# Kernel tuning notes

Hardware: AMD Instinct MI355X
Metric: run time of the kernel (lower is better)

## Reference

```python
import jax, jax.numpy as jnp
import numpy as np

N_NODES = 50000
N_EDGES = 1600000
F_IN = 64
C = 128
NOUT = 3
N_LAYERS = 3  # 1 encoder EGNN + 2 decoder EGNN


def setup_inputs() -> dict:
    key = jax.random.key(0)
    ks = jax.random.split(key, 16)
    s = lambda k, shp, scale: jax.random.normal(k, shp, dtype=jnp.float32) * scale
    inp = {
        'src': jax.random.randint(ks[0], (N_EDGES,), 0, N_NODES),
        'dst': jax.random.randint(ks[1], (N_EDGES,), 0, N_NODES),
        'node_attr': jax.random.normal(ks[2], (N_NODES, F_IN), dtype=jnp.float32),
        'xyz': jax.random.normal(ks[3], (N_NODES, 3), dtype=jnp.float32),
        'emb_w1': s(ks[4], (F_IN, C), F_IN ** -0.5),
        'emb_b1': jnp.zeros((C,), jnp.float32),
        'ln1_g': jnp.ones((C,), jnp.float32),
        'ln1_b': jnp.zeros((C,), jnp.float32),
        'emb_w2': s(ks[5], (C, C), C ** -0.5),
        'emb_b2': jnp.zeros((C,), jnp.float32),
        'ln2_g': jnp.ones((C,), jnp.float32),
        'ln2_b': jnp.zeros((C,), jnp.float32),
        'e_w1': s(ks[6], (N_LAYERS, 2 * C + 1, C), (2 * C + 1) ** -0.5),
        'e_b1': jnp.zeros((N_LAYERS, C), jnp.float32),
        'e_w2': s(ks[7], (N_LAYERS, C, C), C ** -0.5),
        'e_b2': jnp.zeros((N_LAYERS, C), jnp.float32),
        'n_w1': s(ks[8], (N_LAYERS, 2 * C, C), (2 * C) ** -0.5),
        'n_b1': jnp.zeros((N_LAYERS, C), jnp.float32),
        'n_w2': s(ks[9], (N_LAYERS, C, C), C ** -0.5),
        'n_b2': jnp.zeros((N_LAYERS, C), jnp.float32),
        'c_w1': s(ks[10], (N_LAYERS, C, C), C ** -0.5),
        'c_b1': jnp.zeros((N_LAYERS, C), jnp.float32),
        'c_w2': s(ks[11], (N_LAYERS, C, 1), 0.01),  # small coord head as in EGNN practice
        'dec_ln_g': jnp.ones((C,), jnp.float32),
        'dec_ln_b': jnp.zeros((C,), jnp.float32),
        'out_w': s(ks[12], (C, NOUT), C ** -0.5),
        'out_b': jnp.zeros((NOUT,), jnp.float32),
    }
    return inp


def _layer_norm(x, g, b, eps=1e-5):
    mu = x.mean(-1, keepdims=True)
    var = ((x - mu) ** 2).mean(-1, keepdims=True)
    return (x - mu) * jax.lax.rsqrt(var + eps) * g + b


def _egnn_layer(h, x, src, dst, ew1, eb1, ew2, eb2, nw1, nb1, nw2, nb2, cw1, cb1, cw2):
    # DGL EGNNConv: messages src -> dst, sum aggregation.
    n = h.shape[0]
    x_diff = x[src] - x[dst]                               # [E, 3]
    radial = (x_diff * x_diff).sum(-1, keepdims=True)      # [E, 1]
    x_diff = x_diff / (jnp.sqrt(radial) + 1e-30)           # normalized diff
    f = jnp.concatenate([h[src], h[dst], radial], axis=-1)  # [E, 2C+1]
    m = jax.nn.silu(f @ ew1 + eb1)
    m = jax.nn.silu(m @ ew2 + eb2)                          # msg_h [E, C]
    cm = jax.nn.silu(m @ cw1 + cb1) @ cw2                   # [E, 1]
    msg_x = cm * x_diff                                     # [E, 3]
    h_agg = jax.ops.segment_sum(m, dst, num_segments=n)
    x_agg = jax.ops.segment_sum(msg_x, dst, num_segments=n)
    h_new = jnp.concatenate([h, h_agg], axis=-1)
    h_new = jax.nn.silu(h_new @ nw1 + nb1) @ nw2 + nb2
    return h_new, x + x_agg


def reference(src, dst, node_attr, xyz,
              emb_w1, emb_b1, ln1_g, ln1_b, emb_w2, emb_b2, ln2_g, ln2_b,
              e_w1, e_b1, e_w2, e_b2, n_w1, n_b1, n_w2, n_b2,
              c_w1, c_b1, c_w2, dec_ln_g, dec_ln_b, out_w, out_b):
    gelu = lambda t: jax.nn.gelu(t, approximate=False)  # torch nn.GELU default (erf)
    # initial node embedding (eval mode: dropout = identity)
    h = gelu(_layer_norm(node_attr @ emb_w1 + emb_b1, ln1_g, ln1_b))
    h = gelu(_layer_norm(h @ emb_w2 + emb_b2, ln2_g, ln2_b))
    # encoder GraphConv: 1 EGNN layer, coord output discarded
    h, _ = _egnn_layer(h, xyz, src, dst,
                       e_w1[0], e_b1[0], e_w2[0], e_b2[0],
                       n_w1[0], n_b1[0], n_w2[0], n_b2[0],
                       c_w1[0], c_b1[0], c_w2[0])
    # decoder EquivalentTransformer: 2 EGNN layers starting again from xyz
    coord = xyz
    for i in (1, 2):
        h, coord = _egnn_layer(h, coord, src, dst,
                               e_w1[i], e_b1[i], e_w2[i], e_b2[i],
                               n_w1[i], n_b1[i], n_w2[i], n_b2[i],
                               c_w1[i], c_b1[i], c_w2[i])
        h = _layer_norm(gelu(h), dec_ln_g, dec_ln_b)
    return h @ out_w + out_b  # [N, nout]
```

## Files before the change

kernel.cpp:

```cpp
#include <hip/hip_runtime.h>
#include <hip/hip_fp16.h>
#include <math.h>

#define NN 50000
#define NE 1600000
#define CC 128
#define FIN 64

typedef __attribute__((ext_vector_type(8))) _Float16 half8;
typedef __attribute__((ext_vector_type(2))) __fp16 fp16x2;
typedef __attribute__((ext_vector_type(4))) float f32x4;

__device__ __forceinline__ f32x4 mfma16f(half8 a, half8 b, f32x4 c) {
  return __builtin_amdgcn_mfma_f32_16x16x32_f16(a, b, c, 0, 0, 0);
}

__device__ __forceinline__ float silu_f(float x) {
  return x * __builtin_amdgcn_rcpf(1.0f + __expf(-x));
}
__device__ __forceinline__ float gelu_f(float x) { return 0.5f * x * (1.0f + erff(x * 0.7071067811865475f)); }

__device__ __forceinline__ unsigned pkrtz(float a, float b) {
  fp16x2 h = __builtin_amdgcn_cvt_pkrtz(a, b);
  return *(unsigned*)&h;
}

__device__ __forceinline__ float hsum32(float v) {
  v += __shfl_xor(v, 16);
  v += __shfl_xor(v, 8);
  v += __shfl_xor(v, 4);
  v += __shfl_xor(v, 2);
  v += __shfl_xor(v, 1);
  return v;
}

__device__ __forceinline__ float hsum8(float v) {
  v += __shfl_xor(v, 4);
  v += __shfl_xor(v, 2);
  v += __shfl_xor(v, 1);
  return v;
}

__global__ __launch_bounds__(256)
void hist_kernel(const int* __restrict__ dst, int* __restrict__ cnt)
{
  const int i = blockIdx.x * 256 + threadIdx.x;
  if (i < NE) atomicAdd(&cnt[dst[i]], 1);
}

__global__ __launch_bounds__(1024)
void scan_kernel(const int* __restrict__ cnt, int* __restrict__ next)
{
  __shared__ int part[1024];
  const int tid = threadIdx.x;
  const int per = (NN + 1023) / 1024;
  const int base = tid * per;
  int s = 0;
  for (int i = 0; i < per; ++i) {
    const int n = base + i;
    if (n < NN) s += cnt[n];
  }
  part[tid] = s;
  __syncthreads();
  if (tid == 0) {
    int acc = 0;
    for (int i = 0; i < 1024; ++i) { const int t = part[i]; part[i] = acc; acc += t; }
  }
  __syncthreads();
  int off = part[tid];
  for (int i = 0; i < per; ++i) {
    const int n = base + i;
    if (n < NN) { next[n] = off; off += cnt[n]; }
  }
}

__global__ __launch_bounds__(256)
void slot_kernel(const int* __restrict__ dst, int* __restrict__ next, int* __restrict__ perm)
{
  const int i = blockIdx.x * 256 + threadIdx.x;
  if (i < NE) perm[atomicAdd(&next[dst[i]], 1)] = i;
}

__global__ __launch_bounds__(256)
void wt_split(const float* __restrict__ W, __half* __restrict__ Wh, __half* __restrict__ Wl,
              const int K, const int layers, const int strideIn)
{
  const int gid = blockIdx.x * 256 + threadIdx.x;
  if (gid >= layers * 128 * K) return;
  const int l = gid / (128 * K);
  const int rem = gid - l * 128 * K;
  const int n = rem / K;
  const int k = rem - n * K;
  const float w = W[(size_t)l * strideIn + (size_t)k * 128 + n];
  const __half hi = __float2half(w);
  Wh[gid] = hi;
  Wl[gid] = __float2half(w - __half2float(hi));
}

__global__ __launch_bounds__(256)
void pq_kernel(const __half* __restrict__ h_hi,
               const __half* __restrict__ W1h, const __half* __restrict__ W1l,
               const float* __restrict__ eb1, __half* __restrict__ PQ)
{
  __shared__ __align__(16) __half ah[32 * 128];
  const int tid = threadIdx.x;
  const int n0 = blockIdx.x * 32;
  {
    const int row = tid >> 3, sub = tid & 7;
    int n = n0 + row; if (n >= NN) n = NN - 1;
    #pragma unroll
    for (int t = 0; t < 2; ++t) {
      const int c8 = sub * 2 + t;
      const uint4 v = *(const uint4*)(h_hi + (size_t)n * CC + c8 * 8);
      *(uint4*)(ah + row * 128 + ((c8 ^ (row & 15)) * 8)) = v;
    }
  }
  __syncthreads();

  const int lane = tid & 63;
  const int li = lane & 15, quad = lane >> 4;
  const int wv = tid >> 6;
  const int c0 = wv * 32 + li, c1 = c0 + 16;

  f32x4 acc[2][4];
  {
    const float b0 = eb1[c0], b1 = eb1[c1];
    acc[0][0] = acc[1][0] = (f32x4){b0, b0, b0, b0};
    acc[0][1] = acc[1][1] = (f32x4){b1, b1, b1, b1};
    acc[0][2] = acc[1][2] = (f32x4){0, 0, 0, 0};
    acc[0][3] = acc[1][3] = (f32x4){0, 0, 0, 0};
  }
  const __half* bp[4] = { W1h + (size_t)c0 * 256, W1h + (size_t)c1 * 256,
                          W1h + (size_t)c0 * 256 + 128, W1h + (size_t)c1 * 256 + 128 };
  const __half* lp[4] = { W1l + (size_t)c0 * 256, W1l + (size_t)c1 * 256,
                          W1l + (size_t)c0 * 256 + 128, W1l + (size_t)c1 * 256 + 128 };
  #pragma unroll
  for (int ks = 0; ks < 4; ++ks) {
    const int ko = ks * 32 + quad * 8;
    half8 Bh[4], Bl[4];
    #pragma unroll
    for (int o = 0; o < 4; ++o) { Bh[o] = *(const half8*)(bp[o] + ko); Bl[o] = *(const half8*)(lp[o] + ko); }
    #pragma unroll
    for (int mi = 0; mi < 2; ++mi) {
      const half8 A = *(const half8*)(ah + (mi * 16 + li) * 128 + (((ks * 4 + quad) ^ li) * 8));
      #pragma unroll
      for (int o = 0; o < 4; ++o) {
        acc[mi][o] = mfma16f(A, Bh[o], acc[mi][o]);
        acc[mi][o] = mfma16f(A, Bl[o], acc[mi][o]);
      }
    }
  }
  const int cmap[4] = { c0, c1, 128 + c0, 128 + c1 };
  #pragma unroll
  for (int mi = 0; mi < 2; ++mi) {
    #pragma unroll
    for (int r = 0; r < 4; ++r) {
      const int n = n0 + mi * 16 + quad * 4 + r;
      if (n < NN) {
        __half* po = PQ + (size_t)n * 256;
        #pragma unroll
        for (int o = 0; o < 4; ++o) po[cmap[o]] = __float2half(acc[mi][o][r]);
      }
    }
  }
}

template<int COORD>
__global__ __launch_bounds__(512)
void edge_kernel(const int* __restrict__ perm,
                 const int* __restrict__ src, const int* __restrict__ dst,
                 const __half* __restrict__ PQ, const float* __restrict__ xyz,
                 const float* __restrict__ w1rad,
                 const __half* __restrict__ W2h, const __half* __restrict__ W2l,
                 const float* __restrict__ eb2,
                 const __half* __restrict__ W3h, const __half* __restrict__ W3l,
                 const float* __restrict__ cb1, const float* __restrict__ cw2,
                 float* __restrict__ h_agg, float* __restrict__ x_agg)
{
  const int EPB = 128;
  __shared__ __align__(16) unsigned char smem[128 * 132 * 2];
  __shared__ int sidx[EPB], didx[EPB];
  __shared__ float radial[EPB];
  __shared__ float xdn[COORD ? EPB : 1][3];
  __shared__ float sx[COORD ? EPB : 1];
  __shared__ float cw2s[COORD ? 128 : 1];

  __half* ab = (__half*)smem;
  __half* tbuf = (__half*)smem;

  const int tid = threadIdx.x;
  const size_t ebase = (size_t)blockIdx.x * EPB;

  if (tid < EPB) {
    const int e = perm[ebase + tid];
    const int s = src[e], d = dst[e];
    sidx[tid] = s; didx[tid] = d;
    const float* xs = xyz + (size_t)s * 3;
    const float* xd = xyz + (size_t)d * 3;
    const float dx = xs[0] - xd[0], dy = xs[1] - xd[1], dz = xs[2] - xd[2];
    const float r = dx * dx + dy * dy + dz * dz;
    radial[tid] = r;
    if (COORD) {
      const float inv = __builtin_amdgcn_rcpf(sqrtf(r) + 1e-30f);
      xdn[tid][0] = dx * inv; xdn[tid][1] = dy * inv; xdn[tid][2] = dz * inv;
    }
  }
  if (COORD && tid >= 128 && tid < 256) cw2s[tid - 128] = cw2[tid - 128];
  __syncthreads();

  {
    const int e = tid >> 2, q = tid & 3, c = q * 32;
    const float r = radial[e];
    const __half* prow = PQ + (size_t)sidx[e] * 256 + c;
    const __half* qrow = PQ + (size_t)didx[e] * 256 + 128 + c;
    #pragma unroll
    for (int i = 0; i < 4; ++i) {
      union { uint4 u; __half2 h2[4]; } pu, qu;
      pu.u = *(const uint4*)(prow + i * 8);
      qu.u = *(const uint4*)(qrow + i * 8);
      const float4 wa = *(const float4*)(w1rad + c + i * 8);
      const float4 wb = *(const float4*)(w1rad + c + i * 8 + 4);
      const float wf[8] = { wa.x, wa.y, wa.z, wa.w, wb.x, wb.y, wb.z, wb.w };
      float v[8];
      #pragma unroll
      for (int j = 0; j < 4; ++j) {
        const float2 p = __half22float2(pu.h2[j]);
        const float2 qq = __half22float2(qu.h2[j]);
        v[2 * j]     = silu_f(p.x + qq.x + r * wf[2 * j]);
        v[2 * j + 1] = silu_f(p.y + qq.y + r * wf[2 * j + 1]);
      }
      uint4 H;
      H.x = pkrtz(v[0], v[1]); H.y = pkrtz(v[2], v[3]);
      H.z = pkrtz(v[4], v[5]); H.w = pkrtz(v[6], v[7]);
      *(uint4*)(ab + e * 128 + (((q * 4 + i) ^ (e & 15)) * 8)) = H;
    }
  }
  __syncthreads();

  const int lane = tid & 63;
  const int li = lane & 15, quad = lane >> 4;
  const int wv = tid >> 6;
  const int c0 = wv * 16 + li;

  f32x4 mm[8];
  {
    const float b0 = eb2[c0];
    #pragma unroll
    for (int mi = 0; mi < 8; ++mi) mm[mi] = (f32x4){b0, b0, b0, b0};
  }
  {
    const __half* bh0 = W2h + (size_t)c0 * 128 + quad * 8;
    const __half* bl0 = W2l + (size_t)c0 * 128 + quad * 8;
    #pragma unroll
    for (int ks = 0; ks < 4; ++ks) {
      const half8 Bh0 = *(const half8*)(bh0 + ks * 32);
      const half8 Bl0 = *(const half8*)(bl0 + ks * 32);
      #pragma unroll
      for (int mi = 0; mi < 8; ++mi) {
        const half8 A = *(const half8*)(ab + (mi * 16 + li) * 128 + (((ks * 4 + quad) ^ li) * 8));
        mm[mi] = mfma16f(A, Bh0, mm[mi]);
        mm[mi] = mfma16f(A, Bl0, mm[mi]);
      }
    }
  }
  #pragma unroll
  for (int mi = 0; mi < 8; ++mi) {
    #pragma unroll
    for (int r = 0; r < 4; ++r) mm[mi][r] = silu_f(mm[mi][r]);
  }
  __syncthreads();

  if (!COORD) {
    #pragma unroll
    for (int mi = 0; mi < 8; ++mi) {
      #pragma unroll
      for (int r = 0; r < 4; ++r)
        tbuf[(mi * 16 + quad * 4 + r) * 132 + c0] = __float2half(mm[mi][r]);
    }
    __syncthreads();
    const int c = tid & 127, grp = tid >> 7;
    const int j0 = grp * 32, j1 = j0 + 32;
    float ss = 0.0f;
    for (int j = j0; j < j1; ++j) {
      ss += __half2float(tbuf[j * 132 + c]);
      const int dj = didx[j];
      if (j == j1 - 1 || didx[j + 1] != dj) {
        atomicAdd(&h_agg[(size_t)dj * CC + c], ss);
        ss = 0.0f;
      }
    }
  } else {
    #pragma unroll
    for (int mi = 0; mi < 8; ++mi) {
      #pragma unroll
      for (int r = 0; r < 4; ++r) {
        const int row = mi * 16 + quad * 4 + r;
        ab[row * 128 + (((c0 >> 3) ^ (row & 15)) * 8) + (c0 & 7)] = __float2half(mm[mi][r]);
      }
    }
    __syncthreads();
    {
      const int c = tid & 127, grp = tid >> 7;
      const int j0 = grp * 32, j1 = j0 + 32;
      float ss = 0.0f;
      for (int j = j0; j < j1; ++j) {
        ss += __half2float(ab[j * 128 + (((c >> 3) ^ (j & 15)) * 8) + (c & 7)]);
        const int dj = didx[j];
        if (j == j1 - 1 || didx[j + 1] != dj) {
          atomicAdd(&h_agg[(size_t)dj * CC + c], ss);
          ss = 0.0f;
        }
      }
    }
    f32x4 tt[8];
    {
      const float b0 = cb1[c0];
      #pragma unroll
      for (int mi = 0; mi < 8; ++mi) tt[mi] = (f32x4){b0, b0, b0, b0};
    }
    {
      const __half* bh0 = W3h + (size_t)c0 * 128 + quad * 8;
      const __half* bl0 = W3l + (size_t)c0 * 128 + quad * 8;
      #pragma unroll
      for (int ks = 0; ks < 4; ++ks) {
        const half8 Bh0 = *(const half8*)(bh0 + ks * 32);
        const half8 Bl0 = *(const half8*)(bl0 + ks * 32);
        #pragma unroll
        for (int mi = 0; mi < 8; ++mi) {
          const half8 A = *(const half8*)(ab + (mi * 16 + li) * 128 + (((ks * 4 + quad) ^ li) * 8));
          tt[mi] = mfma16f(A, Bh0, tt[mi]);
          tt[mi] = mfma16f(A, Bl0, tt[mi]);
        }
      }
    }
    __syncthreads();
    #pragma unroll
    for (int mi = 0; mi < 8; ++mi) {
      #pragma unroll
      for (int r = 0; r < 4; ++r)
        tbuf[(mi * 16 + quad * 4 + r) * 132 + c0] = __float2half(silu_f(tt[mi][r]));
    }
    __syncthreads();
    if (tid < EPB) {
      float ss = 0.0f;
      #pragma unroll 8
      for (int k = 0; k < CC; ++k) ss += __half2float(tbuf[tid * 132 + k]) * cw2s[k];
      sx[tid] = ss;
    }
    __syncthreads();
    if (tid < 12) {
      const int c = tid >> 2, grp = tid & 3;
      const int j0 = grp * 32, j1 = j0 + 32;
      float a = 0.0f;
      for (int j = j0; j < j1; ++j) {
        a += sx[j] * xdn[j][c];
        const int dj = didx[j];
        if (j == j1 - 1 || didx[j + 1] != dj) {
          atomicAdd(&x_agg[(size_t)dj * 3 + c], a);
          a = 0.0f;
        }
      }
    }
  }
}

__global__ __launch_bounds__(256)
void node_mfma(const __half* __restrict__ h_hi, const __half* __restrict__ h_lo,
               const float* __restrict__ h_agg,
               const __half* __restrict__ NW1h, const __half* __restrict__ NW1l,
               const float* __restrict__ nb1,
               const __half* __restrict__ NW2h, const __half* __restrict__ NW2l,
               const float* __restrict__ nb2,
               __half* __restrict__ ho_hi, __half* __restrict__ ho_lo, const int post_ln,
               const float* __restrict__ lng, const float* __restrict__ lnb,
               const int do_coord, const float* __restrict__ xin,
               const float* __restrict__ x_agg, float* __restrict__ coord_out)
{
  __shared__ __align__(16) __half ab[32 * 256];
  __shared__ __align__(16) __half ab2[32 * 128];
  __shared__ float cbuf[32 * 132];

  const int tid = threadIdx.x;
  const int n0 = blockIdx.x * 32;

  {
    const int row = tid >> 3, q = tid & 7;
    int n = n0 + row; if (n >= NN) n = NN - 1;
    #pragma unroll
    for (int t = 0; t < 2; ++t) {
      const int c8 = q * 2 + t;
      const uint4 v = *(const uint4*)(h_hi + (size_t)n * CC + c8 * 8);
      *(uint4*)(ab + row * 256 + ((c8 ^ (row & 15)) * 8)) = v;
    }
    #pragma unroll
    for (int t = 0; t < 2; ++t) {
      const int c8 = 16 + q * 2 + t;
      const float4 a0 = *(const float4*)(h_agg + (size_t)n * CC + (q * 2 + t) * 8);
      const float4 a1 = *(const float4*)(h_agg + (size_t)n * CC + (q * 2 + t) * 8 + 4);
      uint4 H;
      H.x = pkrtz(a0.x, a0.y); H.y = pkrtz(a0.z, a0.w);
      H.z = pkrtz(a1.x, a1.y); H.w = pkrtz(a1.z, a1.w);
      *(uint4*)(ab + row * 256 + ((c8 ^ (row & 15)) * 8)) = H;
    }
  }
  if (do_coord && tid < 96) {
    const int n = n0 + tid / 3, d = tid % 3;
    if (n < NN)
      coord_out[(size_t)n * 3 + d] = xin[(size_t)n * 3 + d] + x_agg[(size_t)n * 3 + d];
  }
  __syncthreads();

  const int lane = tid & 63;
  const int li = lane & 15, quad = lane >> 4;
  const int wv = tid >> 6;

  f32x4 a1[2][2];
  {
    const float b0 = nb1[wv * 32 + li], b1 = nb1[wv * 32 + 16 + li];
    a1[0][0] = a1[1][0] = (f32x4){b0, b0, b0, b0};
    a1[0][1] = a1[1][1] = (f32x4){b1, b1, b1, b1};
  }
  {
    const __half* b0h = NW1h + (size_t)(wv * 32 + li) * 256 + quad * 8;
    const __half* b0l = NW1l + (size_t)(wv * 32 + li) * 256 + quad * 8;
    const __half* b1h = NW1h + (size_t)(wv * 32 + 16 + li) * 256 + quad * 8;
    const __half* b1l = NW1l + (size_t)(wv * 32 + 16 + li) * 256 + quad * 8;
    #pragma unroll
    for (int ks = 0; ks < 8; ++ks) {
      const half8 Bh0 = *(const half8*)(b0h + ks * 32);
      const half8 Bl0 = *(const half8*)(b0l + ks * 32);
      const half8 Bh1 = *(const half8*)(b1h + ks * 32);
      const half8 Bl1 = *(const half8*)(b1l + ks * 32);
      #pragma unroll
      for (int mi = 0; mi < 2; ++mi) {
        const half8 A = *(const half8*)(ab + (mi * 16 + li) * 256 + (((ks * 4 + quad) ^ li) * 8));
        a1[mi][0] = mfma16f(A, Bh0, a1[mi][0]);
        a1[mi][0] = mfma16f(A, Bl0, a1[mi][0]);
        a1[mi][1] = mfma16f(A, Bh1, a1[mi][1]);
        a1[mi][1] = mfma16f(A, Bl1, a1[mi][1]);
      }
    }
  }
  #pragma unroll
  for (int mi = 0; mi < 2; ++mi) {
    #pragma unroll
    for (int nc = 0; nc < 2; ++nc) {
      const int col = wv * 32 + nc * 16 + li;
      #pragma unroll
      for (int r = 0; r < 4; ++r) {
        const int row = mi * 16 + quad * 4 + r;
        ab2[row * 128 + (((col >> 3) ^ (row & 15)) * 8) + (col & 7)] =
            __float2half(silu_f(a1[mi][nc][r]));
      }
    }
  }
  __syncthreads();

  f32x4 a2[2][2];
  {
    const float b0 = nb2[wv * 32 + li], b1 = nb2[wv * 32 + 16 + li];
    a2[0][0] = a2[1][0] = (f32x4){b0, b0, b0, b0};
    a2[0][1] = a2[1][1] = (f32x4){b1, b1, b1, b1};
  }
  {
    const __half* b0h = NW2h + (size_t)(wv * 32 + li) * 128 + quad * 8;
    const __half* b0l = NW2l + (size_t)(wv * 32 + li) * 128 + quad * 8;
    const __half* b1h = NW2h + (size_t)(wv * 32 + 16 + li) * 128 + quad * 8;
    const __half* b1l = NW2l + (size_t)(wv * 32 + 16 + li) * 128 + quad * 8;
    #pragma unroll
    for (int ks = 0; ks < 4; ++ks) {
      const half8 Bh0 = *(const half8*)(b0h + ks * 32);
      const half8 Bl0 = *(const half8*)(b0l + ks * 32);
      const half8 Bh1 = *(const half8*)(b1h + ks * 32);
      const half8 Bl1 = *(const half8*)(b1l + ks * 32);
      #pragma unroll
      for (int mi = 0; mi < 2; ++mi) {
        const half8 A = *(const half8*)(ab2 + (mi * 16 + li) * 128 + (((ks * 4 + quad) ^ li) * 8));
        a2[mi][0] = mfma16f(A, Bh0, a2[mi][0]);
        a2[mi][0] = mfma16f(A, Bl0, a2[mi][0]);
        a2[mi][1] = mfma16f(A, Bh1, a2[mi][1]);
        a2[mi][1] = mfma16f(A, Bl1, a2[mi][1]);
      }
    }
  }
  #pragma unroll
  for (int mi = 0; mi < 2; ++mi) {
    #pragma unroll
    for (int nc = 0; nc < 2; ++nc) {
      const int col = wv * 32 + nc * 16 + li;
      #pragma unroll
      for (int r = 0; r < 4; ++r)
        cbuf[(mi * 16 + quad * 4 + r) * 132 + col] = a2[mi][nc][r];
    }
  }
  __syncthreads();

  {
    const int row = tid >> 3, q = tid & 7;
    const int n = n0 + row;
    float v[16];
    #pragma unroll
    for (int i = 0; i < 16; ++i) v[i] = cbuf[row * 132 + q * 16 + i];
    if (post_ln) {
      float s = 0.0f;
      #pragma unroll
      for (int i = 0; i < 16; ++i) { v[i] = gelu_f(v[i]); s += v[i]; }
      const float mu = hsum8(s) * (1.0f / 128.0f);
      float vs = 0.0f;
      #pragma unroll
      for (int i = 0; i < 16; ++i) { v[i] -= mu; vs += v[i] * v[i]; }
      const float rs = rsqrtf(hsum8(vs) * (1.0f / 128.0f) + 1e-5f);
      #pragma unroll
      for (int i = 0; i < 16; ++i)
        v[i] = v[i] * rs * lng[q * 16 + i] + lnb[q * 16 + i];
    }
    if (n < NN) {
      __half h[16], l[16];
      #pragma unroll
      for (int i = 0; i < 16; ++i) {
        h[i] = __float2half(v[i]);
        l[i] = __float2half(v[i] - __half2float(h[i]));
      }
      #pragma unroll
      for (int t = 0; t < 2; ++t) {
        *(uint4*)(ho_hi + (size_t)n * CC + q * 16 + t * 8) = *(uint4*)(h + t * 8);
        *(uint4*)(ho_lo + (size_t)n * CC + q * 16 + t * 8) = *(uint4*)(l + t * 8);
      }
    }
  }
}

template<int K, int ROWS>
__device__ __forceinline__ void mm_tile(const float* __restrict__ fb, const int fstride,
                                        const float* __restrict__ W, const float* __restrict__ bias,
                                        const int c0, const int r0, float (&acc)[ROWS][4])
{
  const float4 b = *(const float4*)(bias + c0);
  #pragma unroll
  for (int i = 0; i < ROWS; ++i) { acc[i][0] = b.x; acc[i][1] = b.y; acc[i][2] = b.z; acc[i][3] = b.w; }
  #pragma unroll 2
  for (int k = 0; k < K; k += 4) {
    const float4 w0 = *(const float4*)(W + (size_t)(k + 0) * CC + c0);
    const float4 w1 = *(const float4*)(W + (size_t)(k + 1) * CC + c0);
    const float4 w2 = *(const float4*)(W + (size_t)(k + 2) * CC + c0);
    const float4 w3 = *(const float4*)(W + (size_t)(k + 3) * CC + c0);
    #pragma unroll
    for (int i = 0; i < ROWS; ++i) {
      const float4 f = *(const float4*)(fb + (r0 + i) * fstride + k);
      acc[i][0] += f.x * w0.x + f.y * w1.x + f.z * w2.x + f.w * w3.x;
      acc[i][1] += f.x * w0.y + f.y * w1.y + f.z * w2.y + f.w * w3.y;
      acc[i][2] += f.x * w0.z + f.y * w1.z + f.z * w2.z + f.w * w3.z;
      acc[i][3] += f.x * w0.w + f.y * w1.w + f.z * w2.w + f.w * w3.w;
    }
  }
}

__device__ __forceinline__ void ln_then_gelu(float (&v)[4], const float* __restrict__ g,
                                             const float* __restrict__ b, const int c0)
{
  const float mu = hsum32(v[0] + v[1] + v[2] + v[3]) * (1.0f / 128.0f);
  const float d0 = v[0] - mu, d1 = v[1] - mu, d2 = v[2] - mu, d3 = v[3] - mu;
  const float var = hsum32(d0 * d0 + d1 * d1 + d2 * d2 + d3 * d3) * (1.0f / 128.0f);
  const float rs = rsqrtf(var + 1e-5f);
  const float4 gv = *(const float4*)(g + c0);
  const float4 bv = *(const float4*)(b + c0);
  v[0] = gelu_f(d0 * rs * gv.x + bv.x);
  v[1] = gelu_f(d1 * rs * gv.y + bv.y);
  v[2] = gelu_f(d2 * rs * gv.z + bv.z);
  v[3] = gelu_f(d3 * rs * gv.w + bv.w);
}

__device__ __forceinline__ void store_hilo4(__half* __restrict__ hi, __half* __restrict__ lo,
                                            const float v0, const float v1,
                                            const float v2, const float v3)
{
  __half h[4], l[4];
  h[0] = __float2half(v0); h[1] = __float2half(v1); h[2] = __float2half(v2); h[3] = __float2half(v3);
  l[0] = __float2half(v0 - __half2float(h[0]));
  l[1] = __float2half(v1 - __half2float(h[1]));
  l[2] = __float2half(v2 - __half2float(h[2]));
  l[3] = __float2half(v3 - __half2float(h[3]));
  *(ushort4*)hi = *(ushort4*)h;
  *(ushort4*)lo = *(ushort4*)l;
}

__global__ __launch_bounds__(256)
void embed_kernel(const float* __restrict__ na,
                  const float* __restrict__ w1, const float* __restrict__ b1,
                  const float* __restrict__ g1, const float* __restrict__ be1,
                  const float* __restrict__ w2, const float* __restrict__ b2,
                  const float* __restrict__ g2, const float* __restrict__ be2,
                  __half* __restrict__ ho_hi, __half* __restrict__ ho_lo)
{
  const int AS = 68, MS = 132;
  __shared__ float ain[16 * AS];
  __shared__ float hb[16 * MS];
  const int tid = threadIdx.x;
  const size_t n0 = (size_t)blockIdx.x * 16;
  {
    const int n = tid >> 4, q = tid & 15;
    *(float4*)(ain + n * AS + q * 4) = *(const float4*)(na + (n0 + n) * FIN + q * 4);
  }
  __syncthreads();
  const int cg = tid & 31, ng = tid >> 5;
  const int c0 = cg * 4, m0 = ng * 2;
  float acc[2][4];
  mm_tile<64, 2>(ain, AS, w1, b1, c0, m0, acc);
  #pragma unroll
  for (int i = 0; i < 2; ++i) {
    ln_then_gelu(acc[i], g1, be1, c0);
    *(float4*)(hb + (m0 + i) * MS + c0) = make_float4(acc[i][0], acc[i][1], acc[i][2], acc[i][3]);
  }
  __syncthreads();
  float acc2[2][4];
  mm_tile<128, 2>(hb, MS, w2, b2, c0, m0, acc2);
  #pragma unroll
  for (int i = 0; i < 2; ++i) {
    ln_then_gelu(acc2[i], g2, be2, c0);
    store_hilo4(ho_hi + (n0 + m0 + i) * CC + c0, ho_lo + (n0 + m0 + i) * CC + c0,
                acc2[i][0], acc2[i][1], acc2[i][2], acc2[i][3]);
  }
}

__global__ __launch_bounds__(192)
void out_kernel(const __half* __restrict__ h_hi, const __half* __restrict__ h_lo,
                const float* __restrict__ w, const float* __restrict__ b,
                float* __restrict__ out)
{
  const int gid = blockIdx.x * 192 + threadIdx.x;
  if (gid >= NN * 3) return;
  const int n = gid / 3, j = gid % 3;
  float acc = b[j];
  const __half* hh = h_hi + (size_t)n * CC;
  const __half* hl = h_lo + (size_t)n * CC;
  #pragma unroll 4
  for (int k = 0; k < CC; ++k) acc += (__half2float(hh[k]) + __half2float(hl[k])) * w[k * 3 + j];
  out[gid] = acc;
}

extern "C" void kernel_launch(void* const* d_in, const int* in_sizes, int n_in,
                              void* d_out, int out_size, void* d_ws, size_t ws_size,
                              hipStream_t stream)
{
  (void)in_sizes; (void)n_in; (void)out_size; (void)ws_size;
  const int*   src       = (const int*)d_in[0];
  const int*   dst       = (const int*)d_in[1];
  const float* node_attr = (const float*)d_in[2];
  const float* xyz       = (const float*)d_in[3];
  const float* emb_w1    = (const float*)d_in[4];
  const float* emb_b1    = (const float*)d_in[5];
  const float* ln1_g     = (const float*)d_in[6];
  const float* ln1_b     = (const float*)d_in[7];
  const float* emb_w2    = (const float*)d_in[8];
  const float* emb_b2    = (const float*)d_in[9];
  const float* ln2_g     = (const float*)d_in[10];
  const float* ln2_b     = (const float*)d_in[11];
  const float* e_w1      = (const float*)d_in[12];
  const float* e_b1      = (const float*)d_in[13];
  const float* e_w2      = (const float*)d_in[14];
  const float* e_b2      = (const float*)d_in[15];
  const float* n_w1      = (const float*)d_in[16];
  const float* n_b1      = (const float*)d_in[17];
  const float* n_w2      = (const float*)d_in[18];
  const float* n_b2      = (const float*)d_in[19];
  const float* c_w1      = (const float*)d_in[20];
  const float* c_b1      = (const float*)d_in[21];
  const float* c_w2      = (const float*)d_in[22];
  const float* dec_ln_g  = (const float*)d_in[23];
  const float* dec_ln_b  = (const float*)d_in[24];
  const float* out_w     = (const float*)d_in[25];
  const float* out_b     = (const float*)d_in[26];

  char* wsb = (char*)d_ws;
  float*  h_agg = (float*)wsb;                      wsb += (size_t)NN * CC * 4;
  __half* PQ    = (__half*)wsb;                     wsb += (size_t)NN * 256 * 2;
  float*  x_agg = (float*)wsb;                      wsb += (size_t)NN * 3 * 4;
  float*  coord = (float*)wsb;                      wsb += (size_t)NN * 3 * 4;
  __half* h_hi  = (__half*)wsb;                     wsb += (size_t)NN * CC * 2;
  __half* h_lo  = (__half*)wsb;                     wsb += (size_t)NN * CC * 2;
  __half* W1h   = (__half*)wsb;                     wsb += (size_t)3 * 128 * 256 * 2;
  __half* W1l   = (__half*)wsb;                     wsb += (size_t)3 * 128 * 256 * 2;
  __half* W2h   = (__half*)wsb;                     wsb += (size_t)3 * 128 * 128 * 2;
  __half* W2l   = (__half*)wsb;                     wsb += (size_t)3 * 128 * 128 * 2;
  __half* W3h   = (__half*)wsb;                     wsb += (size_t)128 * 128 * 2;
  __half* W3l   = (__half*)wsb;                     wsb += (size_t)128 * 128 * 2;
  __half* NW1h  = (__half*)wsb;                     wsb += (size_t)3 * 128 * 256 * 2;
  __half* NW1l  = (__half*)wsb;                     wsb += (size_t)3 * 128 * 256 * 2;
  __half* NW2h  = (__half*)wsb;                     wsb += (size_t)3 * 128 * 128 * 2;
  __half* NW2l  = (__half*)wsb;                     wsb += (size_t)3 * 128 * 128 * 2;
  int*    permA = (int*)wsb;                        wsb += (size_t)NE * 4;
  int*    cnt   = (int*)wsb;                        wsb += (size_t)NN * 4;
  int*    nextA = (int*)wsb;                        wsb += (size_t)NN * 4;
  float*  out   = (float*)d_out;

  const int NGRID = NN / 16;
  const int N32GRID = (NN + 31) / 32;
  const int EGRID = NE / 128;

  wt_split<<<(3 * 128 * 256 + 255) / 256, 256, 0, stream>>>(e_w1, W1h, W1l, 256, 3, 257 * 128);
  wt_split<<<(3 * 128 * 128 + 255) / 256, 256, 0, stream>>>(e_w2, W2h, W2l, 128, 3, 128 * 128);
  wt_split<<<(128 * 128 + 255) / 256, 256, 0, stream>>>(c_w1 + (size_t)128 * 128, W3h, W3l, 128, 1, 0);
  wt_split<<<(3 * 128 * 256 + 255) / 256, 256, 0, stream>>>(n_w1, NW1h, NW1l, 256, 3, 256 * 128);
  wt_split<<<(3 * 128 * 128 + 255) / 256, 256, 0, stream>>>(n_w2, NW2h, NW2l, 128, 3, 128 * 128);

  (void)hipMemsetAsync(cnt, 0, (size_t)NN * 4, stream);
  hist_kernel<<<(NE + 255) / 256, 256, 0, stream>>>(dst, cnt);
  scan_kernel<<<1, 1024, 0, stream>>>(cnt, nextA);
  slot_kernel<<<(NE + 255) / 256, 256, 0, stream>>>(dst, nextA, permA);

  embed_kernel<<<NGRID, 256, 0, stream>>>(node_attr, emb_w1, emb_b1, ln1_g, ln1_b,
                                          emb_w2, emb_b2, ln2_g, ln2_b, h_hi, h_lo);

  (void)hipMemsetAsync(h_agg, 0, (size_t)NN * CC * 4, stream);
  pq_kernel<<<N32GRID, 256, 0, stream>>>(h_hi, W1h, W1l, e_b1, PQ);
  edge_kernel<0><<<EGRID, 512, 0, stream>>>(permA, src, dst, PQ, xyz,
      e_w1 + (size_t)256 * CC, W2h, W2l, e_b2, W3h, W3l, c_b1, c_w2, h_agg, x_agg);
  node_mfma<<<N32GRID, 256, 0, stream>>>(h_hi, h_lo, h_agg,
      NW1h, NW1l, n_b1, NW2h, NW2l, n_b2,
      h_hi, h_lo, 0, dec_ln_g, dec_ln_b, 0, xyz, x_agg, coord);

  (void)hipMemsetAsync(h_agg, 0, (size_t)NN * CC * 4, stream);
  (void)hipMemsetAsync(x_agg, 0, (size_t)NN * 3 * 4, stream);
  pq_kernel<<<N32GRID, 256, 0, stream>>>(h_hi, W1h + (size_t)128 * 256,
      W1l + (size_t)128 * 256, e_b1 + CC, PQ);
  edge_kernel<1><<<EGRID, 512, 0, stream>>>(permA, src, dst, PQ, xyz,
      e_w1 + (size_t)(257 + 256) * CC,
      W2h + (size_t)128 * 128, W2l + (size_t)128 * 128, e_b2 + CC,
      W3h, W3l, c_b1 + CC, c_w2 + CC, h_agg, x_agg);
  node_mfma<<<N32GRID, 256, 0, stream>>>(h_hi, h_lo, h_agg,
      NW1h + (size_t)128 * 256, NW1l + (size_t)128 * 256, n_b1 + CC,
      NW2h + (size_t)128 * 128, NW2l + (size_t)128 * 128, n_b2 + CC,
      h_hi, h_lo, 1, dec_ln_g, dec_ln_b, 1, xyz, x_agg, coord);

  (void)hipMemsetAsync(h_agg, 0, (size_t)NN * CC * 4, stream);
  pq_kernel<<<N32GRID, 256, 0, stream>>>(h_hi, W1h + (size_t)2 * 128 * 256,
      W1l + (size_t)2 * 128 * 256, e_b1 + 2 * CC, PQ);
  edge_kernel<0><<<EGRID, 512, 0, stream>>>(permA, src, dst, PQ, coord,
      e_w1 + (size_t)(2 * 257 + 256) * CC,
      W2h + (size_t)2 * 128 * 128, W2l + (size_t)2 * 128 * 128, e_b2 + 2 * CC,
      W3h, W3l, c_b1, c_w2, h_agg, x_agg);
  node_mfma<<<N32GRID, 256, 0, stream>>>(h_hi, h_lo, h_agg,
      NW1h + (size_t)2 * 128 * 256, NW1l + (size_t)2 * 128 * 256, n_b1 + 2 * CC,
      NW2h + (size_t)2 * 128 * 128, NW2l + (size_t)2 * 128 * 128, n_b2 + 2 * CC,
      h_hi, h_lo, 1, dec_ln_g, dec_ln_b, 0, xyz, x_agg, coord);

  out_kernel<<<(NN * 3 + 191) / 192, 192, 0, stream>>>(h_hi, h_lo, out_w, out_b, out);
}
```

Before: 1.786 ms.

## Store sorted src/dst pairs directly and double edge tile to 256 per block

The slot kernel now writes (src,dst) int2 pairs in dst-sorted order instead of a permutation, so edge kernels read indices contiguously rather than through an indirect gather of src/dst. The edge kernel also processes 256 edges per 1024-thread block, with two wave groups each covering 128 rows, which doubles shared memory per block and widens segmented-reduction runs before atomics. The larger blocks cut the number of atomic flushes but may lower occupancy, since LDS use per block roughly doubles.

```diff
diff --git a/kernel.cpp b/kernel.cpp
--- a/kernel.cpp
+++ b/kernel.cpp
@@ -75,10 +75,14 @@
 }
 
 __global__ __launch_bounds__(256)
-void slot_kernel(const int* __restrict__ dst, int* __restrict__ next, int* __restrict__ perm)
+void slot_kernel(const int* __restrict__ src, const int* __restrict__ dst,
+                 int* __restrict__ next, int2* __restrict__ sd)
 {
   const int i = blockIdx.x * 256 + threadIdx.x;
-  if (i < NE) perm[atomicAdd(&next[dst[i]], 1)] = i;
+  if (i < NE) {
+    const int d = dst[i];
+    sd[atomicAdd(&next[d], 1)] = make_int2(src[i], d);
+  }
 }
 
 __global__ __launch_bounds__(256)
@@ -166,9 +170,8 @@
 }
 
 template<int COORD>
-__global__ __launch_bounds__(512)
-void edge_kernel(const int* __restrict__ perm,
-                 const int* __restrict__ src, const int* __restrict__ dst,
+__global__ __launch_bounds__(1024)
+void edge_kernel(const int2* __restrict__ sd,
                  const __half* __restrict__ PQ, const float* __restrict__ xyz,
                  const float* __restrict__ w1rad,
                  const __half* __restrict__ W2h, const __half* __restrict__ W2l,
@@ -177,8 +180,8 @@
                  const float* __restrict__ cb1, const float* __restrict__ cw2,
                  float* __restrict__ h_agg, float* __restrict__ x_agg)
 {
-  const int EPB = 128;
-  __shared__ __align__(16) unsigned char smem[128 * 132 * 2];
+  const int EPB = 256;
+  __shared__ __align__(16) unsigned char smem[256 * 132 * 2];
   __shared__ int sidx[EPB], didx[EPB];
   __shared__ float radial[EPB];
   __shared__ float xdn[COORD ? EPB : 1][3];
@@ -192,8 +195,8 @@
   const size_t ebase = (size_t)blockIdx.x * EPB;
 
   if (tid < EPB) {
-    const int e = perm[ebase + tid];
-    const int s = src[e], d = dst[e];
+    const int2 p = sd[ebase + tid];
+    const int s = p.x, d = p.y;
     sidx[tid] = s; didx[tid] = d;
     const float* xs = xyz + (size_t)s * 3;
     const float* xd = xyz + (size_t)d * 3;
@@ -205,7 +208,7 @@
       xdn[tid][0] = dx * inv; xdn[tid][1] = dy * inv; xdn[tid][2] = dz * inv;
     }
   }
-  if (COORD && tid >= 128 && tid < 256) cw2s[tid - 128] = cw2[tid - 128];
+  if (COORD && tid >= 256 && tid < 384) cw2s[tid - 256] = cw2[tid - 256];
   __syncthreads();
 
   {
@@ -240,7 +243,8 @@
   const int lane = tid & 63;
   const int li = lane & 15, quad = lane >> 4;
   const int wv = tid >> 6;
-  const int c0 = wv * 16 + li;
+  const int mh = wv >> 3;
+  const int c0 = (wv & 7) * 16 + li;
 
   f32x4 mm[8];
   {
@@ -257,7 +261,8 @@
       const half8 Bl0 = *(const half8*)(bl0 + ks * 32);
       #pragma unroll
       for (int mi = 0; mi < 8; ++mi) {
-        const half8 A = *(const half8*)(ab + (mi * 16 + li) * 128 + (((ks * 4 + quad) ^ li) * 8));
+        const int row = mh * 128 + mi * 16 + li;
+        const half8 A = *(const half8*)(ab + row * 128 + (((ks * 4 + quad) ^ li) * 8));
         mm[mi] = mfma16f(A, Bh0, mm[mi]);
         mm[mi] = mfma16f(A, Bl0, mm[mi]);
       }
@@ -275,7 +280,7 @@
     for (int mi = 0; mi < 8; ++mi) {
       #pragma unroll
       for (int r = 0; r < 4; ++r)
-        tbuf[(mi * 16 + quad * 4 + r) * 132 + c0] = __float2half(mm[mi][r]);
+        tbuf[(mh * 128 + mi * 16 + quad * 4 + r) * 132 + c0] = __float2half(mm[mi][r]);
     }
     __syncthreads();
     const int c = tid & 127, grp = tid >> 7;
@@ -294,7 +299,7 @@
     for (int mi = 0; mi < 8; ++mi) {
       #pragma unroll
       for (int r = 0; r < 4; ++r) {
-        const int row = mi * 16 + quad * 4 + r;
+        const int row = mh * 128 + mi * 16 + quad * 4 + r;
         ab[row * 128 + (((c0 >> 3) ^ (row & 15)) * 8) + (c0 & 7)] = __float2half(mm[mi][r]);
       }
     }
@@ -327,7 +332,8 @@
         const half8 Bl0 = *(const half8*)(bl0 + ks * 32);
         #pragma unroll
         for (int mi = 0; mi < 8; ++mi) {
-          const half8 A = *(const half8*)(ab + (mi * 16 + li) * 128 + (((ks * 4 + quad) ^ li) * 8));
+          const int row = mh * 128 + mi * 16 + li;
+          const half8 A = *(const half8*)(ab + row * 128 + (((ks * 4 + quad) ^ li) * 8));
           tt[mi] = mfma16f(A, Bh0, tt[mi]);
           tt[mi] = mfma16f(A, Bl0, tt[mi]);
         }
@@ -338,7 +344,7 @@
     for (int mi = 0; mi < 8; ++mi) {
       #pragma unroll
       for (int r = 0; r < 4; ++r)
-        tbuf[(mi * 16 + quad * 4 + r) * 132 + c0] = __float2half(silu_f(tt[mi][r]));
+        tbuf[(mh * 128 + mi * 16 + quad * 4 + r) * 132 + c0] = __float2half(silu_f(tt[mi][r]));
     }
     __syncthreads();
     if (tid < EPB) {
@@ -348,8 +354,8 @@
       sx[tid] = ss;
     }
     __syncthreads();
-    if (tid < 12) {
-      const int c = tid >> 2, grp = tid & 3;
+    if (tid < 24) {
+      const int c = tid >> 3, grp = tid & 7;
       const int j0 = grp * 32, j1 = j0 + 32;
       float a = 0.0f;
       for (int j = j0; j < j1; ++j) {
@@ -688,14 +694,14 @@
   __half* NW1l  = (__half*)wsb;                     wsb += (size_t)3 * 128 * 256 * 2;
   __half* NW2h  = (__half*)wsb;                     wsb += (size_t)3 * 128 * 128 * 2;
   __half* NW2l  = (__half*)wsb;                     wsb += (size_t)3 * 128 * 128 * 2;
-  int*    permA = (int*)wsb;                        wsb += (size_t)NE * 4;
+  int2*   sdA   = (int2*)wsb;                       wsb += (size_t)NE * 8;
   int*    cnt   = (int*)wsb;                        wsb += (size_t)NN * 4;
   int*    nextA = (int*)wsb;                        wsb += (size_t)NN * 4;
   float*  out   = (float*)d_out;
 
   const int NGRID = NN / 16;
   const int N32GRID = (NN + 31) / 32;
-  const int EGRID = NE / 128;
+  const int EGRID = NE / 256;
 
   wt_split<<<(3 * 128 * 256 + 255) / 256, 256, 0, stream>>>(e_w1, W1h, W1l, 256, 3, 257 * 128);
   wt_split<<<(3 * 128 * 128 + 255) / 256, 256, 0, stream>>>(e_w2, W2h, W2l, 128, 3, 128 * 128);
@@ -706,14 +712,14 @@
   (void)hipMemsetAsync(cnt, 0, (size_t)NN * 4, stream);
   hist_kernel<<<(NE + 255) / 256, 256, 0, stream>>>(dst, cnt);
   scan_kernel<<<1, 1024, 0, stream>>>(cnt, nextA);
-  slot_kernel<<<(NE + 255) / 256, 256, 0, stream>>>(dst, nextA, permA);
+  slot_kernel<<<(NE + 255) / 256, 256, 0, stream>>>(src, dst, nextA, sdA);
 
   embed_kernel<<<NGRID, 256, 0, stream>>>(node_attr, emb_w1, emb_b1, ln1_g, ln1_b,
                                           emb_w2, emb_b2, ln2_g, ln2_b, h_hi, h_lo);
 
   (void)hipMemsetAsync(h_agg, 0, (size_t)NN * CC * 4, stream);
   pq_kernel<<<N32GRID, 256, 0, stream>>>(h_hi, W1h, W1l, e_b1, PQ);
-  edge_kernel<0><<<EGRID, 512, 0, stream>>>(permA, src, dst, PQ, xyz,
+  edge_kernel<0><<<EGRID, 1024, 0, stream>>>(sdA, PQ, xyz,
       e_w1 + (size_t)256 * CC, W2h, W2l, e_b2, W3h, W3l, c_b1, c_w2, h_agg, x_agg);
   node_mfma<<<N32GRID, 256, 0, stream>>>(h_hi, h_lo, h_agg,
       NW1h, NW1l, n_b1, NW2h, NW2l, n_b2,
@@ -723,7 +729,7 @@
   (void)hipMemsetAsync(x_agg, 0, (size_t)NN * 3 * 4, stream);
   pq_kernel<<<N32GRID, 256, 0, stream>>>(h_hi, W1h + (size_t)128 * 256,
       W1l + (size_t)128 * 256, e_b1 + CC, PQ);
-  edge_kernel<1><<<EGRID, 512, 0, stream>>>(permA, src, dst, PQ, xyz,
+  edge_kernel<1><<<EGRID, 1024, 0, stream>>>(sdA, PQ, xyz,
       e_w1 + (size_t)(257 + 256) * CC,
       W2h + (size_t)128 * 128, W2l + (size_t)128 * 128, e_b2 + CC,
       W3h, W3l, c_b1 + CC, c_w2 + CC, h_agg, x_agg);
@@ -735,7 +741,7 @@
   (void)hipMemsetAsync(h_agg, 0, (size_t)NN * CC * 4, stream);
   pq_kernel<<<N32GRID, 256, 0, stream>>>(h_hi, W1h + (size_t)2 * 128 * 256,
       W1l + (size_t)2 * 128 * 256, e_b1 + 2 * CC, PQ);
-  edge_kernel<0><<<EGRID, 512, 0, stream>>>(permA, src, dst, PQ, coord,
+  edge_kernel<0><<<EGRID, 1024, 0, stream>>>(sdA, PQ, coord,
       e_w1 + (size_t)(2 * 257 + 256) * CC,
       W2h + (size_t)2 * 128 * 128, W2l + (size_t)2 * 128 * 128, e_b2 + 2 * CC,
       W3h, W3l, c_b1, c_w2, h_agg, x_agg);
```

New measurement: 2.117 ms. +18.6%, slower.
